# Optimization experiments

Measured on AMD Instinct MI355X. Metric: run time of the kernel, lower is better.

## Reference

```python
import jax, jax.numpy as jnp
import numpy as np

NUM_GROUPS = 32
EPS = 1e-5


def setup_inputs() -> dict:
    key = jax.random.key(0)
    ks = jax.random.split(key, 4)
    B, C, H, W = 4, 256, 64, 64
    x = jax.random.normal(ks[0], (B, C, H, W), dtype=jnp.float32)
    norm_w = jnp.ones((C,), dtype=jnp.float32)
    norm_b = jnp.zeros((C,), dtype=jnp.float32)
    qkv_w = jax.random.normal(ks[1], (3 * C, C), dtype=jnp.float32) * (C ** -0.5)
    qkv_b = jnp.zeros((3 * C,), dtype=jnp.float32)
    proj_w = jax.random.normal(ks[2], (C, C), dtype=jnp.float32) * (C ** -0.5)
    proj_b = jnp.zeros((C,), dtype=jnp.float32)
    return {"x": x, "norm_w": norm_w, "norm_b": norm_b, "qkv_w": qkv_w,
            "qkv_b": qkv_b, "proj_w": proj_w, "proj_b": proj_b, "num_heads": 1}


def _group_norm(x, w, b):
    B, C, H, W = x.shape
    xg = x.reshape(B, NUM_GROUPS, C // NUM_GROUPS, H, W)
    mean = xg.mean(axis=(2, 3, 4), keepdims=True)
    var = xg.var(axis=(2, 3, 4), keepdims=True)
    xn = ((xg - mean) * jax.lax.rsqrt(var + EPS)).reshape(B, C, H, W)
    return xn * w[None, :, None, None] + b[None, :, None, None]


def reference(x, norm_w, norm_b, qkv_w, qkv_b, proj_w, proj_b, num_heads):
    B, C, H, W = x.shape
    N = H * W
    d = C // num_heads
    xn = _group_norm(x, norm_w, norm_b)
    # 1x1 conv == channel matmul: [B,3C,H,W]
    qkv = jnp.einsum('oc,bchw->bohw', qkv_w, xn) + qkv_b[None, :, None, None]
    qkv = qkv.reshape(B, 3, num_heads, d, N)
    q, k, v = qkv[:, 0], qkv[:, 1], qkv[:, 2]  # each [B,h,d,N]
    scale = d ** -0.5
    attn = jnp.einsum('bhdi,bhdj->bhij', q, k) * scale  # [B,h,N,N]
    attn = jax.nn.softmax(attn, axis=-1)
    out = jnp.einsum('bhij,bhdj->bhdi', attn, v)  # [B,h,d,N]
    out = out.reshape(B, C, H, W)
    out = jnp.einsum('oc,bchw->bohw', proj_w, out) + proj_b[None, :, None, None]
    return x + out
```

## Files before the change

### kernel.cpp

```cpp
#include <hip/hip_runtime.h>
#include <stdint.h>
#include <stddef.h>

#define NB 4
#define NC 256
#define NSP 4096
#define NG 32
#define CPG 8
#define GEPS 1e-5f
#define SCALE 0.0625f
#define SCALE_L2E 0.090168440f
#define NROWS (NB * NSP)
#define JSPLIT 4

typedef __attribute__((ext_vector_type(8))) short s8v;
typedef __attribute__((ext_vector_type(4))) float f4v;
typedef __attribute__((ext_vector_type(16))) float f16v;
typedef __attribute__((ext_vector_type(4))) unsigned short us4v;
typedef __attribute__((ext_vector_type(4))) unsigned int u4v;

__device__ __forceinline__ float b2f(unsigned short h) {
  union { unsigned u; float f; } x; x.u = ((unsigned)h) << 16; return x.f;
}
__device__ __forceinline__ unsigned short f2b(float f) {
  union { float f; unsigned u; } x; x.f = f;
  unsigned r = x.u + 0x7fffu + ((x.u >> 16) & 1u);
  return (unsigned short)(r >> 16);
}
__device__ __forceinline__ unsigned packbf(float lo, float hi) {
  union { float f; unsigned u; } a, b; a.f = lo; b.f = hi;
  return (b.u & 0xffff0000u) | (a.u >> 16);
}

__global__ __launch_bounds__(256) void cvt2_kernel(
    const float* __restrict__ qw, const float* __restrict__ pw,
    unsigned short* __restrict__ wq, unsigned short* __restrict__ wp) {
  int i = (blockIdx.x * 256 + threadIdx.x) * 4;
  const float* src; unsigned short* dst; int j;
  if (i < 3 * NC * NC) { src = qw; dst = wq; j = i; }
  else { src = pw; dst = wp; j = i - 3 * NC * NC; }
  float4 v = *(const float4*)(src + j);
  us4v p;
  p[0] = f2b(v.x); p[1] = f2b(v.y); p[2] = f2b(v.z); p[3] = f2b(v.w);
  *(us4v*)(dst + j) = p;
}

__global__ __launch_bounds__(256) void gn_kernel(
    const float* __restrict__ x, const float* __restrict__ w,
    const float* __restrict__ bias, unsigned short* __restrict__ xn) {
  int b = blockIdx.x >> 5;
  int g = blockIdx.x & 31;
  const float* xp = x + ((size_t)b * NC + (size_t)g * CPG) * NSP;
  int t = threadIdx.x;
  float s = 0.f, ss = 0.f;
  for (int i = 4 * t; i < CPG * NSP; i += 1024) {
    float4 v = *(const float4*)(xp + i);
    s += v.x + v.y + v.z + v.w;
    ss += v.x * v.x + v.y * v.y + v.z * v.z + v.w * v.w;
  }
  __shared__ float r1[256], r2[256];
  r1[t] = s; r2[t] = ss;
  __syncthreads();
  for (int off = 128; off > 0; off >>= 1) {
    if (t < off) { r1[t] += r1[t + off]; r2[t] += r2[t + off]; }
    __syncthreads();
  }
  float mean = r1[0] * (1.f / (CPG * NSP));
  float var  = r2[0] * (1.f / (CPG * NSP)) - mean * mean;
  float rstd = rsqrtf(var + GEPS);
  float wv[CPG], bv[CPG];
  for (int c = 0; c < CPG; c++) {
    wv[c] = w[g * CPG + c] * rstd;
    bv[c] = bias[g * CPG + c] - mean * wv[c];
  }
  for (int n = t; n < NSP; n += 256) {
    s8v pk;
    for (int c = 0; c < CPG; c++) {
      float v = xp[(size_t)c * NSP + n];
      ((unsigned short*)&pk)[c] = f2b(v * wv[c] + bv[c]);
    }
    *(s8v*)(xn + ((size_t)(b * NSP + n) * NC + g * CPG)) = pk;
  }
}

__global__ __launch_bounds__(256) void qkv_gemm(
    const unsigned short* __restrict__ W, const unsigned short* __restrict__ xnG,
    const float* __restrict__ qkvb,
    unsigned short* __restrict__ q, unsigned short* __restrict__ k,
    unsigned short* __restrict__ v) {
  const int sec = blockIdx.y >> 1;
  const int m0 = (blockIdx.y & 1) * 128;
  const int n0 = blockIdx.x * 128;
  const unsigned short* A  = W + (size_t)sec * NC * NC;
  const unsigned short* Bt = xnG + (size_t)blockIdx.z * NSP * NC;
  unsigned short* dst = (sec == 0 ? q : (sec == 1 ? k : v)) + (size_t)blockIdx.z * NSP * NC;
  const float scl = (sec == 0) ? SCALE_L2E : 1.f;

  __shared__ unsigned short As[128 * 32], Bs[128 * 32];
  const int t = threadIdx.x;
  const int lane = t & 63, wave = t >> 6;
  const int wm = (wave >> 1) * 64, wn = (wave & 1) * 64;
  const int l16 = lane & 15, quad = lane >> 4;
  const int srow = t >> 2, skc = (t & 3) * 8;

  f4v acc[4][4];
  for (int mi = 0; mi < 4; mi++)
    for (int ni = 0; ni < 4; ni++)
      acc[mi][ni] = (f4v){0.f, 0.f, 0.f, 0.f};

  const unsigned short* Ag0 = A  + (size_t)(m0 + srow) * NC + skc;
  const unsigned short* Ag1 = A  + (size_t)(m0 + srow + 64) * NC + skc;
  const unsigned short* Bg0 = Bt + (size_t)(n0 + srow) * NC + skc;
  const unsigned short* Bg1 = Bt + (size_t)(n0 + srow + 64) * NC + skc;

  for (int k0 = 0; k0 < NC; k0 += 32) {
    s8v a0 = *(const s8v*)(Ag0 + k0);
    s8v a1 = *(const s8v*)(Ag1 + k0);
    s8v b0 = *(const s8v*)(Bg0 + k0);
    s8v b1 = *(const s8v*)(Bg1 + k0);
    __syncthreads();
    *(s8v*)(As + srow * 32 + skc) = a0;
    *(s8v*)(As + (srow + 64) * 32 + skc) = a1;
    *(s8v*)(Bs + srow * 32 + skc) = b0;
    *(s8v*)(Bs + (srow + 64) * 32 + skc) = b1;
    __syncthreads();
    s8v af[4], bfr[4];
    for (int mi = 0; mi < 4; mi++)
      af[mi] = *(const s8v*)(As + (wm + mi * 16 + l16) * 32 + quad * 8);
    for (int ni = 0; ni < 4; ni++)
      bfr[ni] = *(const s8v*)(Bs + (wn + ni * 16 + l16) * 32 + quad * 8);
    for (int mi = 0; mi < 4; mi++)
      for (int ni = 0; ni < 4; ni++)
        acc[mi][ni] = __builtin_amdgcn_mfma_f32_16x16x32_bf16(af[mi], bfr[ni], acc[mi][ni], 0, 0, 0);
  }

  for (int mi = 0; mi < 4; mi++) {
    const int rb = m0 + wm + mi * 16 + quad * 4;
    for (int ni = 0; ni < 4; ni++) {
      const int col = n0 + wn + ni * 16 + l16;
      f4v a = acc[mi][ni];
      if (sec < 2) {
        us4v pk;
        for (int r = 0; r < 4; r++)
          pk[r] = f2b((a[r] + qkvb[sec * NC + rb + r]) * scl);
        const size_t off = (size_t)(col >> 5) * 8192 + (rb >> 4) * 512 +
                           ((rb >> 3) & 1) * 256 + (col & 31) * 8 + (rb & 7);
        *(us4v*)(dst + off) = pk;
      } else {
        for (int r = 0; r < 4; r++) {
          const int d = rb + r;
          const size_t off = (size_t)(col >> 5) * 8192 + (d >> 5) * 1024 +
                             ((col >> 4) & 1) * 512 + ((col >> 3) & 1) * 256 +
                             (d & 31) * 8 + (col & 7);
          dst[off] = f2b(a[r] + qkvb[2 * NC + d]);
        }
      }
    }
  }
}

__global__ __launch_bounds__(256, 2) void flash10_kernel(
    const unsigned short* __restrict__ q, const unsigned short* __restrict__ k,
    const unsigned short* __restrict__ v, unsigned short* __restrict__ Opart,
    float* __restrict__ Lpart) {
  const int qt = blockIdx.x, b = blockIdx.y, js = blockIdx.z;
  const size_t sNC = (size_t)NSP * NC;
  const unsigned short* qb = q + b * sNC;
  const unsigned short* kb = k + b * sNC;
  const unsigned short* vb = v + b * sNC;
  const int t = threadIdx.x, lane = t & 63, w = t >> 6;

  __shared__ unsigned short K_lds[2][16 * 512];
  __shared__ unsigned short V_lds[2][16 * 512];

  f16v zero16;
  #pragma unroll
  for (int r = 0; r < 16; r++) zero16[r] = 0.f;

  s8v qf[16];
  {
    const unsigned short* qp = qb + (size_t)(qt * 4 + w) * 8192 + lane * 8;
    #pragma unroll
    for (int kc = 0; kc < 16; kc++)
      qf[kc] = *(const s8v*)(qp + kc * 512);
  }

  f16v accO[8];
  #pragma unroll
  for (int dt = 0; dt < 8; dt++) accO[dt] = zero16;
  float l4[4] = {0.f, 0.f, 0.f, 0.f};

  const int jbeg = js * (NSP / JSPLIT);
  const int NT = (NSP / JSPLIT) / 32;

  auto stage = [&](int j0, int bufsel) {
    const size_t tb = (size_t)(j0 >> 5) * 16;
    #pragma unroll
    for (int ii = 0; ii < 8; ii++) {
      const int idx = w * 8 + ii;
      const unsigned short* gp;
      unsigned short* ld;
      if (idx < 16) {
        gp = kb + (tb + idx) * 512 + lane * 8;
        ld = &K_lds[bufsel][idx * 512];
      } else {
        const int dt = idx - 16;
        gp = vb + (tb + dt) * 512 + lane * 8;
        ld = &V_lds[bufsel][dt * 512];
      }
      __builtin_amdgcn_global_load_lds(
          (const __attribute__((address_space(1))) unsigned int*)gp,
          (__attribute__((address_space(3))) unsigned int*)ld, 16, 0, 0);
    }
  };

  stage(jbeg, 0);
  for (int jt = 0; jt < NT; jt++) {
    __syncthreads();
    if (jt + 1 < NT) stage(jbeg + (jt + 1) * 32, (jt + 1) & 1);
    const unsigned short* Kc = K_lds[jt & 1];
    const unsigned short* Vc = V_lds[jt & 1];

    f16v accS = zero16;
    __builtin_amdgcn_s_setprio(1);
    #pragma unroll
    for (int kc = 0; kc < 16; kc++) {
      s8v kf = *(const s8v*)(Kc + kc * 512 + lane * 8);
      accS = __builtin_amdgcn_mfma_f32_32x32x16_bf16(kf, qf[kc], accS, 0, 0, 0);
    }
    __builtin_amdgcn_s_setprio(0);

    float p[16];
    #pragma unroll
    for (int r = 0; r < 16; r++) {
      p[r] = exp2f(accS[r]);
      l4[r & 3] += p[r];
    }

    u4v pw0, pw1;
    {
      unsigned a0 = packbf(p[0], p[1]),   b0 = packbf(p[4], p[5]);
      asm("v_permlane32_swap_b32 %0, %1" : "+v"(a0), "+v"(b0));
      unsigned a1 = packbf(p[2], p[3]),   b1 = packbf(p[6], p[7]);
      asm("v_permlane32_swap_b32 %0, %1" : "+v"(a1), "+v"(b1));
      unsigned a2 = packbf(p[8], p[9]),   b2 = packbf(p[12], p[13]);
      asm("v_permlane32_swap_b32 %0, %1" : "+v"(a2), "+v"(b2));
      unsigned a3 = packbf(p[10], p[11]), b3 = packbf(p[14], p[15]);
      asm("v_permlane32_swap_b32 %0, %1" : "+v"(a3), "+v"(b3));
      pw0[0] = a0; pw0[1] = a1; pw0[2] = b0; pw0[3] = b1;
      pw1[0] = a2; pw1[1] = a3; pw1[2] = b2; pw1[3] = b3;
    }
    const s8v pb0 = __builtin_bit_cast(s8v, pw0);
    const s8v pb1 = __builtin_bit_cast(s8v, pw1);

    __builtin_amdgcn_s_setprio(1);
    #pragma unroll
    for (int dt = 0; dt < 8; dt++) {
      s8v vf0 = *(const s8v*)(Vc + dt * 1024 + lane * 8);
      s8v vf1 = *(const s8v*)(Vc + dt * 1024 + 512 + lane * 8);
      accO[dt] = __builtin_amdgcn_mfma_f32_32x32x16_bf16(vf0, pb0, accO[dt], 0, 0, 0);
      accO[dt] = __builtin_amdgcn_mfma_f32_32x32x16_bf16(vf1, pb1, accO[dt], 0, 0, 0);
    }
    __builtin_amdgcn_s_setprio(0);
  }

  float l_acc = l4[0] + l4[1] + l4[2] + l4[3];
  const float ltot = l_acc + __shfl_xor(l_acc, 32, 64);
  const int qrow = b * NSP + qt * 128 + w * 32 + (lane & 31);
  if (lane < 32)
    Lpart[(size_t)js * NROWS + qrow] = ltot;

  unsigned short* Op = Opart + ((size_t)js * NROWS + qrow) * NC;
  const int hi = lane >> 5;
  #pragma unroll
  for (int dt = 0; dt < 8; dt++) {
    #pragma unroll
    for (int g = 0; g < 4; g++) {
      us4v pk;
      #pragma unroll
      for (int r = 0; r < 4; r++)
        pk[r] = f2b(accO[dt][g * 4 + r]);
      *(us4v*)(Op + dt * 32 + g * 8 + hi * 4) = pk;
    }
  }
}

__global__ __launch_bounds__(256) void proj_gemm(
    const unsigned short* __restrict__ Wp, const unsigned short* __restrict__ Opart,
    const float* __restrict__ Lpart, const float* __restrict__ pb,
    const float* __restrict__ x, float* __restrict__ out) {
  const int z = blockIdx.z, m0 = blockIdx.y * 128, n0 = blockIdx.x * 128;
  __shared__ unsigned short As[128 * 32], Bs[128 * 32];
  const int t = threadIdx.x;
  const int lane = t & 63, wave = t >> 6;
  const int wm = (wave >> 1) * 64, wn = (wave & 1) * 64;
  const int l16 = lane & 15, quad = lane >> 4;
  const int srow = t >> 2, skc = (t & 3) * 8;

  const int prow0 = z * NSP + n0 + srow;
  const int prow1 = prow0 + 64;
  float ls0 = 0.f, ls1 = 0.f;
  for (int js = 0; js < JSPLIT; js++) {
    ls0 += Lpart[(size_t)js * NROWS + prow0];
    ls1 += Lpart[(size_t)js * NROWS + prow1];
  }
  const float inv0 = 1.f / ls0, inv1 = 1.f / ls1;

  f4v acc[4][4];
  for (int mi = 0; mi < 4; mi++)
    for (int ni = 0; ni < 4; ni++)
      acc[mi][ni] = (f4v){0.f, 0.f, 0.f, 0.f};

  const unsigned short* Ag0 = Wp + (size_t)(m0 + srow) * NC + skc;
  const unsigned short* Ag1 = Wp + (size_t)(m0 + srow + 64) * NC + skc;

  for (int k0 = 0; k0 < NC; k0 += 32) {
    s8v a0 = *(const s8v*)(Ag0 + k0);
    s8v a1 = *(const s8v*)(Ag1 + k0);
    float bv0[8], bv1[8];
    for (int e = 0; e < 8; e++) { bv0[e] = 0.f; bv1[e] = 0.f; }
    for (int js = 0; js < JSPLIT; js++) {
      const s8v o0 = *(const s8v*)(Opart + ((size_t)js * NROWS + prow0) * NC + k0 + skc);
      const s8v o1 = *(const s8v*)(Opart + ((size_t)js * NROWS + prow1) * NC + k0 + skc);
      for (int e = 0; e < 8; e++) {
        bv0[e] += b2f(((const unsigned short*)&o0)[e]);
        bv1[e] += b2f(((const unsigned short*)&o1)[e]);
      }
    }
    s8v b0, b1;
    for (int e = 0; e < 8; e++) {
      ((unsigned short*)&b0)[e] = f2b(bv0[e] * inv0);
      ((unsigned short*)&b1)[e] = f2b(bv1[e] * inv1);
    }
    __syncthreads();
    *(s8v*)(As + srow * 32 + skc) = a0;
    *(s8v*)(As + (srow + 64) * 32 + skc) = a1;
    *(s8v*)(Bs + srow * 32 + skc) = b0;
    *(s8v*)(Bs + (srow + 64) * 32 + skc) = b1;
    __syncthreads();
    s8v af[4], bfr[4];
    for (int mi = 0; mi < 4; mi++)
      af[mi] = *(const s8v*)(As + (wm + mi * 16 + l16) * 32 + quad * 8);
    for (int ni = 0; ni < 4; ni++)
      bfr[ni] = *(const s8v*)(Bs + (wn + ni * 16 + l16) * 32 + quad * 8);
    for (int mi = 0; mi < 4; mi++)
      for (int ni = 0; ni < 4; ni++)
        acc[mi][ni] = __builtin_amdgcn_mfma_f32_16x16x32_bf16(af[mi], bfr[ni], acc[mi][ni], 0, 0, 0);
  }

  float* C = out + (size_t)z * NC * NSP;
  const float* R = x + (size_t)z * NC * NSP;
  for (int mi = 0; mi < 4; mi++) {
    const int rb = m0 + wm + mi * 16 + quad * 4;
    for (int ni = 0; ni < 4; ni++) {
      const int col = n0 + wn + ni * 16 + l16;
      f4v a = acc[mi][ni];
      for (int r = 0; r < 4; r++)
        C[(size_t)(rb + r) * NSP + col] =
            a[r] + pb[rb + r] + R[(size_t)(rb + r) * NSP + col];
    }
  }
}

extern "C" void kernel_launch(void* const* d_in, const int* in_sizes, int n_in,
                              void* d_out, int out_size, void* d_ws, size_t ws_size,
                              hipStream_t stream) {
  const float* x      = (const float*)d_in[0];
  const float* norm_w = (const float*)d_in[1];
  const float* norm_b = (const float*)d_in[2];
  const float* qkv_w  = (const float*)d_in[3];
  const float* qkv_b  = (const float*)d_in[4];
  const float* proj_w = (const float*)d_in[5];
  const float* proj_b = (const float*)d_in[6];
  float* out = (float*)d_out;

  char* ws = (char*)d_ws;
  unsigned short* wq = (unsigned short*)ws;
  unsigned short* wp = (unsigned short*)(ws + 3 * NC * NC * 2);
  char* wst = ws + (1 << 20);
  const size_t szBNC = (size_t)NB * NSP * NC * 2;
  unsigned short* xn = (unsigned short*)wst;
  unsigned short* q  = (unsigned short*)(wst + szBNC);
  unsigned short* k  = (unsigned short*)(wst + 2 * szBNC);
  unsigned short* v  = (unsigned short*)(wst + 3 * szBNC);
  unsigned short* Opart = (unsigned short*)(wst + 4 * szBNC);
  float* Lpart = (float*)(wst + 4 * szBNC + (size_t)JSPLIT * NROWS * NC * 2);

  cvt2_kernel<<<dim3(4 * NC * NC / 1024), 256, 0, stream>>>(qkv_w, proj_w, wq, wp);
  gn_kernel<<<dim3(NB * NG), 256, 0, stream>>>(x, norm_w, norm_b, xn);
  qkv_gemm<<<dim3(NSP / 128, 6, NB), 256, 0, stream>>>(wq, xn, qkv_b, q, k, v);
  flash10_kernel<<<dim3(NSP / 128, NB, JSPLIT), 256, 0, stream>>>(q, k, v, Opart, Lpart);
  proj_gemm<<<dim3(NSP / 128, NC / 128, NB), 256, 0, stream>>>(
      wp, Opart, Lpart, proj_b, x, out);
}
```

Before: 214.1 us.

## Fuse weight conversion into GEMMs, cache group in LDS, drop setprio

Removes the separate weight-conversion kernel; both GEMMs now read fp32 weights and convert them to bf16 inline while loading tiles. The group-norm kernel moves to 512 threads and keeps the whole group slab in LDS (128 KB), so the second pass reads shared memory instead of global memory. The flash kernel drops its s_setprio hints and switches from exp2f with a log2e-prescaled q to __expf with a plain scale. The trade-offs are extra fp32 weight traffic and conversion work in every GEMM block, and a large LDS footprint that limits group-norm occupancy.

```diff
diff --git a/kernel.cpp b/kernel.cpp
--- a/kernel.cpp
+++ b/kernel.cpp
@@ -9,7 +9,6 @@
 #define CPG 8
 #define GEPS 1e-5f
 #define SCALE 0.0625f
-#define SCALE_L2E 0.090168440f
 #define NROWS (NB * NSP)
 #define JSPLIT 4
 
@@ -27,41 +26,48 @@
   unsigned r = x.u + 0x7fffu + ((x.u >> 16) & 1u);
   return (unsigned short)(r >> 16);
 }
+__device__ __forceinline__ unsigned short f2b_rtz(float f) {
+  union { float f; unsigned u; } x; x.f = f;
+  return (unsigned short)(x.u >> 16);
+}
 __device__ __forceinline__ unsigned packbf(float lo, float hi) {
   union { float f; unsigned u; } a, b; a.f = lo; b.f = hi;
   return (b.u & 0xffff0000u) | (a.u >> 16);
 }
-
-__global__ __launch_bounds__(256) void cvt2_kernel(
-    const float* __restrict__ qw, const float* __restrict__ pw,
-    unsigned short* __restrict__ wq, unsigned short* __restrict__ wp) {
-  int i = (blockIdx.x * 256 + threadIdx.x) * 4;
-  const float* src; unsigned short* dst; int j;
-  if (i < 3 * NC * NC) { src = qw; dst = wq; j = i; }
-  else { src = pw; dst = wp; j = i - 3 * NC * NC; }
-  float4 v = *(const float4*)(src + j);
-  us4v p;
-  p[0] = f2b(v.x); p[1] = f2b(v.y); p[2] = f2b(v.z); p[3] = f2b(v.w);
-  *(us4v*)(dst + j) = p;
-}
-
-__global__ __launch_bounds__(256) void gn_kernel(
+__device__ __forceinline__ s8v pack8(float4 lo, float4 hi) {
+  s8v r;
+  ((unsigned short*)&r)[0] = f2b(lo.x);
+  ((unsigned short*)&r)[1] = f2b(lo.y);
+  ((unsigned short*)&r)[2] = f2b(lo.z);
+  ((unsigned short*)&r)[3] = f2b(lo.w);
+  ((unsigned short*)&r)[4] = f2b(hi.x);
+  ((unsigned short*)&r)[5] = f2b(hi.y);
+  ((unsigned short*)&r)[6] = f2b(hi.z);
+  ((unsigned short*)&r)[7] = f2b(hi.w);
+  return r;
+}
+
+__global__ __launch_bounds__(512) void gn_kernel(
     const float* __restrict__ x, const float* __restrict__ w,
     const float* __restrict__ bias, unsigned short* __restrict__ xn) {
   int b = blockIdx.x >> 5;
   int g = blockIdx.x & 31;
   const float* xp = x + ((size_t)b * NC + (size_t)g * CPG) * NSP;
   int t = threadIdx.x;
+
+  __shared__ float xs[CPG * NSP];
+  __shared__ float r1[512], r2[512];
+
   float s = 0.f, ss = 0.f;
-  for (int i = 4 * t; i < CPG * NSP; i += 1024) {
+  for (int i = 4 * t; i < CPG * NSP; i += 2048) {
     float4 v = *(const float4*)(xp + i);
+    *(float4*)(xs + i) = v;
     s += v.x + v.y + v.z + v.w;
     ss += v.x * v.x + v.y * v.y + v.z * v.z + v.w * v.w;
   }
-  __shared__ float r1[256], r2[256];
   r1[t] = s; r2[t] = ss;
   __syncthreads();
-  for (int off = 128; off > 0; off >>= 1) {
+  for (int off = 256; off > 0; off >>= 1) {
     if (t < off) { r1[t] += r1[t + off]; r2[t] += r2[t + off]; }
     __syncthreads();
   }
@@ -73,10 +79,10 @@
     wv[c] = w[g * CPG + c] * rstd;
     bv[c] = bias[g * CPG + c] - mean * wv[c];
   }
-  for (int n = t; n < NSP; n += 256) {
+  for (int n = t; n < NSP; n += 512) {
     s8v pk;
     for (int c = 0; c < CPG; c++) {
-      float v = xp[(size_t)c * NSP + n];
+      float v = xs[c * NSP + n];
       ((unsigned short*)&pk)[c] = f2b(v * wv[c] + bv[c]);
     }
     *(s8v*)(xn + ((size_t)(b * NSP + n) * NC + g * CPG)) = pk;
@@ -84,17 +90,17 @@
 }
 
 __global__ __launch_bounds__(256) void qkv_gemm(
-    const unsigned short* __restrict__ W, const unsigned short* __restrict__ xnG,
+    const float* __restrict__ Wf, const unsigned short* __restrict__ xnG,
     const float* __restrict__ qkvb,
     unsigned short* __restrict__ q, unsigned short* __restrict__ k,
     unsigned short* __restrict__ v) {
   const int sec = blockIdx.y >> 1;
   const int m0 = (blockIdx.y & 1) * 128;
   const int n0 = blockIdx.x * 128;
-  const unsigned short* A  = W + (size_t)sec * NC * NC;
+  const float* A = Wf + (size_t)sec * NC * NC;
   const unsigned short* Bt = xnG + (size_t)blockIdx.z * NSP * NC;
   unsigned short* dst = (sec == 0 ? q : (sec == 1 ? k : v)) + (size_t)blockIdx.z * NSP * NC;
-  const float scl = (sec == 0) ? SCALE_L2E : 1.f;
+  const float scl = (sec == 0) ? SCALE : 1.f;
 
   __shared__ unsigned short As[128 * 32], Bs[128 * 32];
   const int t = threadIdx.x;
@@ -108,14 +114,14 @@
     for (int ni = 0; ni < 4; ni++)
       acc[mi][ni] = (f4v){0.f, 0.f, 0.f, 0.f};
 
-  const unsigned short* Ag0 = A  + (size_t)(m0 + srow) * NC + skc;
-  const unsigned short* Ag1 = A  + (size_t)(m0 + srow + 64) * NC + skc;
+  const float* Ag0 = A + (size_t)(m0 + srow) * NC + skc;
+  const float* Ag1 = A + (size_t)(m0 + srow + 64) * NC + skc;
   const unsigned short* Bg0 = Bt + (size_t)(n0 + srow) * NC + skc;
   const unsigned short* Bg1 = Bt + (size_t)(n0 + srow + 64) * NC + skc;
 
   for (int k0 = 0; k0 < NC; k0 += 32) {
-    s8v a0 = *(const s8v*)(Ag0 + k0);
-    s8v a1 = *(const s8v*)(Ag1 + k0);
+    s8v a0 = pack8(*(const float4*)(Ag0 + k0), *(const float4*)(Ag0 + k0 + 4));
+    s8v a1 = pack8(*(const float4*)(Ag1 + k0), *(const float4*)(Ag1 + k0 + 4));
     s8v b0 = *(const s8v*)(Bg0 + k0);
     s8v b1 = *(const s8v*)(Bg1 + k0);
     __syncthreads();
@@ -159,7 +165,7 @@
   }
 }
 
-__global__ __launch_bounds__(256, 2) void flash10_kernel(
+__global__ __launch_bounds__(256, 2) void flash11_kernel(
     const unsigned short* __restrict__ q, const unsigned short* __restrict__ k,
     const unsigned short* __restrict__ v, unsigned short* __restrict__ Opart,
     float* __restrict__ Lpart) {
@@ -222,18 +228,16 @@
     const unsigned short* Vc = V_lds[jt & 1];
 
     f16v accS = zero16;
-    __builtin_amdgcn_s_setprio(1);
     #pragma unroll
     for (int kc = 0; kc < 16; kc++) {
       s8v kf = *(const s8v*)(Kc + kc * 512 + lane * 8);
       accS = __builtin_amdgcn_mfma_f32_32x32x16_bf16(kf, qf[kc], accS, 0, 0, 0);
     }
-    __builtin_amdgcn_s_setprio(0);
 
     float p[16];
     #pragma unroll
     for (int r = 0; r < 16; r++) {
-      p[r] = exp2f(accS[r]);
+      p[r] = __expf(accS[r]);
       l4[r & 3] += p[r];
     }
 
@@ -253,7 +257,6 @@
     const s8v pb0 = __builtin_bit_cast(s8v, pw0);
     const s8v pb1 = __builtin_bit_cast(s8v, pw1);
 
-    __builtin_amdgcn_s_setprio(1);
     #pragma unroll
     for (int dt = 0; dt < 8; dt++) {
       s8v vf0 = *(const s8v*)(Vc + dt * 1024 + lane * 8);
@@ -261,7 +264,6 @@
       accO[dt] = __builtin_amdgcn_mfma_f32_32x32x16_bf16(vf0, pb0, accO[dt], 0, 0, 0);
       accO[dt] = __builtin_amdgcn_mfma_f32_32x32x16_bf16(vf1, pb1, accO[dt], 0, 0, 0);
     }
-    __builtin_amdgcn_s_setprio(0);
   }
 
   float l_acc = l4[0] + l4[1] + l4[2] + l4[3];
@@ -286,7 +288,7 @@
 }
 
 __global__ __launch_bounds__(256) void proj_gemm(
-    const unsigned short* __restrict__ Wp, const unsigned short* __restrict__ Opart,
+    const float* __restrict__ Wpf, const unsigned short* __restrict__ Opart,
     const float* __restrict__ Lpart, const float* __restrict__ pb,
     const float* __restrict__ x, float* __restrict__ out) {
   const int z = blockIdx.z, m0 = blockIdx.y * 128, n0 = blockIdx.x * 128;
@@ -311,12 +313,12 @@
     for (int ni = 0; ni < 4; ni++)
       acc[mi][ni] = (f4v){0.f, 0.f, 0.f, 0.f};
 
-  const unsigned short* Ag0 = Wp + (size_t)(m0 + srow) * NC + skc;
-  const unsigned short* Ag1 = Wp + (size_t)(m0 + srow + 64) * NC + skc;
+  const float* Ag0 = Wpf + (size_t)(m0 + srow) * NC + skc;
+  const float* Ag1 = Wpf + (size_t)(m0 + srow + 64) * NC + skc;
 
   for (int k0 = 0; k0 < NC; k0 += 32) {
-    s8v a0 = *(const s8v*)(Ag0 + k0);
-    s8v a1 = *(const s8v*)(Ag1 + k0);
+    s8v a0 = pack8(*(const float4*)(Ag0 + k0), *(const float4*)(Ag0 + k0 + 4));
+    s8v a1 = pack8(*(const float4*)(Ag1 + k0), *(const float4*)(Ag1 + k0 + 4));
     float bv0[8], bv1[8];
     for (int e = 0; e < 8; e++) { bv0[e] = 0.f; bv1[e] = 0.f; }
     for (int js = 0; js < JSPLIT; js++) {
@@ -375,8 +377,6 @@
   float* out = (float*)d_out;
 
   char* ws = (char*)d_ws;
-  unsigned short* wq = (unsigned short*)ws;
-  unsigned short* wp = (unsigned short*)(ws + 3 * NC * NC * 2);
   char* wst = ws + (1 << 20);
   const size_t szBNC = (size_t)NB * NSP * NC * 2;
   unsigned short* xn = (unsigned short*)wst;
@@ -386,10 +386,9 @@
   unsigned short* Opart = (unsigned short*)(wst + 4 * szBNC);
   float* Lpart = (float*)(wst + 4 * szBNC + (size_t)JSPLIT * NROWS * NC * 2);
 
-  cvt2_kernel<<<dim3(4 * NC * NC / 1024), 256, 0, stream>>>(qkv_w, proj_w, wq, wp);
-  gn_kernel<<<dim3(NB * NG), 256, 0, stream>>>(x, norm_w, norm_b, xn);
-  qkv_gemm<<<dim3(NSP / 128, 6, NB), 256, 0, stream>>>(wq, xn, qkv_b, q, k, v);
-  flash10_kernel<<<dim3(NSP / 128, NB, JSPLIT), 256, 0, stream>>>(q, k, v, Opart, Lpart);
+  gn_kernel<<<dim3(NB * NG), 512, 0, stream>>>(x, norm_w, norm_b, xn);
+  qkv_gemm<<<dim3(NSP / 128, 6, NB), 256, 0, stream>>>(qkv_w, xn, qkv_b, q, k, v);
+  flash11_kernel<<<dim3(NSP / 128, NB, JSPLIT), 256, 0, stream>>>(q, k, v, Opart, Lpart);
   proj_gemm<<<dim3(NSP / 128, NC / 128, NB), 256, 0, stream>>>(
-      wp, Opart, Lpart, proj_b, x, out);
-}
+      proj_w, Opart, Lpart, proj_b, x, out);
+}
```

Result: no change. 210.3 us (-1.8%).
